# Performance work log

Hardware: AMD Instinct MI355X
Metric: run time of the kernel (lower is better)

## Reference

```python
import jax, jax.numpy as jnp
import numpy as np

B, TOPK, MN = 128, 32, 64
MAX_NODES, H, E = 256, 128, 128
N_ENT, N_REL = 40000, 400


def setup_inputs() -> dict:
    key = jax.random.key(0)
    ks = jax.random.split(key, 11)
    s = 0.02  # weight init scale
    return {
        "node_embeddings": jax.random.normal(ks[0], (B, MAX_NODES + 2, H), jnp.float32),
        "entity_table": jax.random.normal(ks[1], (N_ENT, E), jnp.float32) * s,
        "relation_table": jax.random.normal(ks[2], (N_REL, E), jnp.float32) * s,
        "W_ih": jax.random.normal(ks[3], (3 * H, 2 * E), jnp.float32) * s,
        "W_hh": jax.random.normal(ks[4], (3 * H, H), jnp.float32) * s,
        "b_ih": jax.random.normal(ks[5], (3 * H,), jnp.float32) * s,
        "b_hh": jax.random.normal(ks[6], (3 * H,), jnp.float32) * s,
        "aim_nodes": jax.random.randint(ks[7], (B, TOPK), 0, MAX_NODES),
        "aim_entities": jax.random.randint(ks[8], (B, TOPK), 0, N_ENT),
        "neighbors": jax.random.randint(ks[9], (B, TOPK, MN, 2), 0, MAX_NODES + 2),
        "neighbors_num": jax.random.randint(ks[10], (B, TOPK), 0, MN + 1),
    }


def reference(node_embeddings, entity_table, relation_table, W_ih, W_hh, b_ih, b_hh,
              aim_nodes, aim_entities, neighbors, neighbors_num):
    # Agent.aggregate with use_rnn=True; returns updated node_embeddings.
    b, topk, mn, _ = neighbors.shape
    h_dim = node_embeddings.shape[-1]
    nb_nodes = neighbors[..., 0]      # (B, topk, mn) node positions
    nb_rel = neighbors[..., 1]        # (B, topk, mn) relation ids

    # per-batch gather of hidden states of neighbor nodes -> (B, topk, mn, H)
    h = jnp.take_along_axis(node_embeddings,
                            nb_nodes.reshape(b, topk * mn)[:, :, None],
                            axis=1).reshape(b, topk, mn, h_dim)
    ent = entity_table[aim_entities]          # (B, topk, E)
    rel = relation_table[nb_rel]              # (B, topk, mn, E)
    # GRU input: concat(aim entity embedding broadcast over neighbors, relation emb)
    x = jnp.concatenate(
        [jnp.broadcast_to(ent[:, :, None, :], rel.shape), rel], axis=-1)  # (B,topk,mn,2E)

    # torch GRUCell: gates ordered (r, z, n)
    gi = jnp.einsum('btme,ge->btmg', x, W_ih) + b_ih  # (B,topk,mn,3H)
    gh = jnp.einsum('btmh,gh->btmg', h, W_hh) + b_hh
    i_r, i_z, i_n = jnp.split(gi, 3, axis=-1)
    h_r, h_z, h_n = jnp.split(gh, 3, axis=-1)
    r = jax.nn.sigmoid(i_r + h_r)
    z = jax.nn.sigmoid(i_z + h_z)
    n = jnp.tanh(i_n + r * h_n)
    h_new = (1.0 - z) * n + z * h              # (B,topk,mn,H)

    # masked mean over valid neighbors (masked_fill(0) then sum / max(num,1))
    mask = jnp.arange(mn)[None, None, :] < neighbors_num[:, :, None]
    denom = neighbors_num.astype(h_new.dtype) + (neighbors_num == 0).astype(h_new.dtype)
    upd = jnp.where(mask[..., None], h_new, 0.0).sum(axis=2) / denom[..., None]  # (B,topk,H)

    # scatter updated representations back into the node table
    bidx = jnp.arange(b)[:, None]
    return node_embeddings.at[bidx, aim_nodes].set(upd)
```

## Files before the change

### kernel.cpp

```cpp
#include <hip/hip_runtime.h>

#define BB     128
#define TOPK   32
#define MN     64
#define NODES  258
#define HD     128
#define G3     384
#define NREL   400
#define SEG1_OFF 512
#define SEG2_OFF 4608
#define NROWS_TOT 37632
#define ROWPAD   37632
#define COLSPLIT 3

typedef __bf16 bf16x8 __attribute__((ext_vector_type(8)));
typedef float  f32x4  __attribute__((ext_vector_type(4)));

__device__ inline unsigned short f2bf(float f) {
    unsigned u = __float_as_uint(f);
    u = (u + 0x7fff + ((u >> 16) & 1)) >> 16;
    return (unsigned short)u;
}
__device__ inline float bf2f(unsigned short s) {
    return __uint_as_float(((unsigned)s) << 16);
}
__device__ inline float fsig(float x) {
    float e = __builtin_amdgcn_exp2f(-1.442695041f * x);
    return __builtin_amdgcn_rcpf(1.f + e);
}
__device__ inline float ftanh(float x) {
    x = fminf(15.f, fmaxf(-15.f, x));
    float e = __builtin_amdgcn_exp2f(2.885390082f * x);
    return (e - 1.f) * __builtin_amdgcn_rcpf(e + 1.f);
}

__global__ __launch_bounds__(256) void pack_all(
        const float* __restrict__ node_emb, const float* __restrict__ ent_tab,
        const float* __restrict__ rel_tab, const int* __restrict__ aim_ent,
        unsigned short* __restrict__ A, unsigned short* __restrict__ NE16,
        float* __restrict__ out) {
    int i = blockIdx.x * 256 + threadIdx.x;
    int row = i >> 4, kc = (i & 15) << 3;
    float4 v0 = {0.f,0.f,0.f,0.f}, v1 = {0.f,0.f,0.f,0.f};
    bool isnode = false;
    int n = 0;
    if (row < NREL) {
        const float4* p = (const float4*)(rel_tab + (size_t)row * 128 + kc);
        v0 = p[0]; v1 = p[1];
    } else if (row < SEG1_OFF) {
    } else if (row < SEG2_OFF) {
        const float* e = ent_tab + (size_t)aim_ent[row - SEG1_OFF] * 128 + kc;
        v0 = ((const float4*)e)[0]; v1 = ((const float4*)e)[1];
    } else {
        isnode = true;
        n = row - SEG2_OFF;
        const float4* p = (const float4*)(node_emb + (size_t)n * 128 + kc);
        v0 = p[0]; v1 = p[1];
        float4* o = (float4*)(out + (size_t)n * 128 + kc);
        o[0] = v0; o[1] = v1;
    }
    union { unsigned short s[8]; uint4 v; } u;
    u.s[0]=f2bf(v0.x); u.s[1]=f2bf(v0.y); u.s[2]=f2bf(v0.z); u.s[3]=f2bf(v0.w);
    u.s[4]=f2bf(v1.x); u.s[5]=f2bf(v1.y); u.s[6]=f2bf(v1.z); u.s[7]=f2bf(v1.w);
    *(uint4*)(A + (size_t)row * 128 + kc) = u.v;
    if (isnode) *(uint4*)(NE16 + (size_t)n * 128 + kc) = u.v;
}

__global__ __launch_bounds__(256) void pack_w(
        const float* __restrict__ W_ih, const float* __restrict__ W_hh,
        const float* __restrict__ b_ih, const float* __restrict__ b_hh,
        unsigned short* __restrict__ Wpack, float* __restrict__ biasb) {
    int i = blockIdx.x * 256 + threadIdx.x;
    int s = i / 49152, r = i % 49152;
    int n = r >> 7, k = r & 127;
    float v;
    if (s == 0)      v = W_ih[n * 256 + 128 + k];
    else if (s == 1) v = W_ih[n * 256 + k];
    else             v = W_hh[n * 128 + k];
    Wpack[i] = f2bf(v);
    if (i < 3 * 384) {
        int s2 = i / 384, g = i % 384;
        biasb[i] = (s2 == 0) ? 0.f : (s2 == 1 ? b_ih[g] : b_hh[g]);
    }
}

__global__ __launch_bounds__(256) void mfma_gemm(
        const unsigned short* __restrict__ A, const unsigned short* __restrict__ Wpack,
        const float* __restrict__ biasb, unsigned short* __restrict__ G) {
    __shared__ __align__(16) unsigned short Bs[128 * 128];
    const int tid = threadIdx.x;
    const int w = tid >> 6, lane = tid & 63;
    const int rb = blockIdx.x / COLSPLIT, cs = blockIdx.x % COLSPLIT;
    const int brow = rb * 128;
    const int row0 = brow + w * 32;
    const int seg  = (brow < SEG1_OFF) ? 0 : (brow < SEG2_OFF ? 1 : 2);
    const int limit = (seg == 0) ? NREL : NROWS_TOT;
    const int colbase = cs * 128;
    const unsigned short* Wt = Wpack + (size_t)seg * 49152 + (size_t)colbase * 128;

#pragma unroll
    for (int ii = 0; ii < 8; ++ii) {
        int dst = ii * 256 + tid;
        int g = dst >> 6, rem = dst & 63;
        int qq = rem >> 4, cc = rem & 15;
        int tt = g >> 2, kbb = g & 3;
        uint4 v = *(const uint4*)(Wt + (size_t)(tt * 16 + cc) * 128 + kbb * 32 + qq * 8);
        *(uint4*)(Bs + dst * 8) = v;
    }

    const int q = lane >> 4, c = lane & 15;
    const int koff = q << 3;
    bf16x8 a0[4], a1[4];
    {
        const unsigned short* Ar0 = A + (size_t)(row0 + c) * 128 + koff;
        const unsigned short* Ar1 = Ar0 + 16 * 128;
#pragma unroll
        for (int kb = 0; kb < 4; ++kb) {
            a0[kb] = *(const bf16x8*)(Ar0 + kb * 32);
            a1[kb] = *(const bf16x8*)(Ar1 + kb * 32);
        }
    }
    float bv[8];
#pragma unroll
    for (int t = 0; t < 8; ++t)
        bv[t] = biasb[seg * 384 + colbase + t * 16 + c];

    __syncthreads();

    const int r0 = row0 + q * 4, r1 = r0 + 16;
#pragma unroll 2
    for (int t = 0; t < 8; ++t) {
        bf16x8 bf[4];
#pragma unroll
        for (int kb = 0; kb < 4; ++kb)
            bf[kb] = *(const bf16x8*)(Bs + (size_t)((t * 4 + kb) * 64 + lane) * 8);
        f32x4 acc0 = {0.f,0.f,0.f,0.f}, acc1 = {0.f,0.f,0.f,0.f};
#pragma unroll
        for (int kb = 0; kb < 4; ++kb) {
            acc0 = __builtin_amdgcn_mfma_f32_16x16x32_bf16(a0[kb], bf[kb], acc0, 0, 0, 0);
            acc1 = __builtin_amdgcn_mfma_f32_16x16x32_bf16(a1[kb], bf[kb], acc1, 0, 0, 0);
        }
        const int gc = colbase + t * 16 + c;
#pragma unroll
        for (int i2 = 0; i2 < 4; ++i2) {
            if (r0 + i2 < limit) G[(size_t)(r0 + i2) * 384 + gc] = f2bf(acc0[i2] + bv[t]);
            if (r1 + i2 < limit) G[(size_t)(r1 + i2) * 384 + gc] = f2bf(acc1[i2] + bv[t]);
        }
    }
}

__global__ __launch_bounds__(512) void gru_agg(
        const unsigned short* __restrict__ NE16, const unsigned short* __restrict__ G,
        const int* __restrict__ aim_nodes, const int* __restrict__ neighbors,
        const int* __restrict__ nb_num, float* __restrict__ out) {
    const int bt = blockIdx.x;
    const int b = bt >> 5, t = bt & 31;
    const int tid = threadIdx.x;
    const int h = tid & 127, j = tid >> 7;

    const int myaim = aim_nodes[bt];
    for (int t2 = t + 1; t2 < TOPK; ++t2)
        if (aim_nodes[b * TOPK + t2] == myaim) return;

    __shared__ int2 nbs[MN];
    __shared__ float part[4][128];
    if (tid < MN) nbs[tid] = ((const int2*)(neighbors + (size_t)bt * MN * 2))[tid];
    __syncthreads();

    const size_t erow = (size_t)(SEG1_OFF + bt) * 384;
    const float ge_r = bf2f(G[erow + h]);
    const float ge_z = bf2f(G[erow + 128 + h]);
    const float ge_n = bf2f(G[erow + 256 + h]);

    int num = nb_num[bt];
    num = (num < 0) ? 0 : (num > MN ? MN : num);

    const unsigned short* ghb = G + (size_t)(SEG2_OFF + b * NODES) * 384;
    const unsigned short* heb = NE16 + (size_t)b * NODES * 128;

    float acc = 0.f;
    int m = j;
    for (; m + 4 < num; m += 8) {
        int2 p0 = nbs[m], p1 = nbs[m + 4];
        const unsigned short* gr0 = G + (size_t)p0.y * 384;
        const unsigned short* gh0 = ghb + (size_t)p0.x * 384;
        const unsigned short* gr1 = G + (size_t)p1.y * 384;
        const unsigned short* gh1 = ghb + (size_t)p1.x * 384;
        float ar0 = bf2f(gr0[h]), az0 = bf2f(gr0[128+h]), an0 = bf2f(gr0[256+h]);
        float hr0 = bf2f(gh0[h]), hz0 = bf2f(gh0[128+h]), hn0 = bf2f(gh0[256+h]);
        float hv0 = bf2f(heb[(size_t)p0.x * 128 + h]);
        float ar1 = bf2f(gr1[h]), az1 = bf2f(gr1[128+h]), an1 = bf2f(gr1[256+h]);
        float hr1 = bf2f(gh1[h]), hz1 = bf2f(gh1[128+h]), hn1 = bf2f(gh1[256+h]);
        float hv1 = bf2f(heb[(size_t)p1.x * 128 + h]);
        float r0 = fsig(ge_r + ar0 + hr0);
        float z0 = fsig(ge_z + az0 + hz0);
        float n0 = ftanh(ge_n + an0 + r0 * hn0);
        acc += (1.f - z0) * n0 + z0 * hv0;
        float r1 = fsig(ge_r + ar1 + hr1);
        float z1 = fsig(ge_z + az1 + hz1);
        float n1 = ftanh(ge_n + an1 + r1 * hn1);
        acc += (1.f - z1) * n1 + z1 * hv1;
    }
    if (m < num) {
        int2 p = nbs[m];
        const unsigned short* gr = G + (size_t)p.y * 384;
        const unsigned short* gh = ghb + (size_t)p.x * 384;
        float r = fsig(ge_r + bf2f(gr[h]) + bf2f(gh[h]));
        float z = fsig(ge_z + bf2f(gr[128 + h]) + bf2f(gh[128 + h]));
        float n = ftanh(ge_n + bf2f(gr[256 + h]) + r * bf2f(gh[256 + h]));
        acc += (1.f - z) * n + z * bf2f(heb[(size_t)p.x * 128 + h]);
    }
    part[j][h] = acc;
    __syncthreads();
    if (j == 0) {
        float s = part[0][h] + part[1][h] + part[2][h] + part[3][h];
        const float denom = (num > 0) ? (float)num : 1.f;
        out[((size_t)b * NODES + myaim) * 128 + h] = s * __builtin_amdgcn_rcpf(denom);
    }
}

extern "C" void kernel_launch(void* const* d_in, const int* in_sizes, int n_in,
                              void* d_out, int out_size, void* d_ws, size_t ws_size,
                              hipStream_t stream) {
    const float* node_emb = (const float*)d_in[0];
    const float* ent_tab  = (const float*)d_in[1];
    const float* rel_tab  = (const float*)d_in[2];
    const float* W_ih     = (const float*)d_in[3];
    const float* W_hh     = (const float*)d_in[4];
    const float* b_ih     = (const float*)d_in[5];
    const float* b_hh     = (const float*)d_in[6];
    const int* aim_nodes  = (const int*)d_in[7];
    const int* aim_ent    = (const int*)d_in[8];
    const int* neighbors  = (const int*)d_in[9];
    const int* nb_num     = (const int*)d_in[10];
    float* out = (float*)d_out;

    unsigned short* G     = (unsigned short*)d_ws;
    unsigned short* A     = G + (size_t)NROWS_TOT * 384;
    unsigned short* NE16  = A + (size_t)ROWPAD * 128;
    unsigned short* Wpack = NE16 + (size_t)BB * NODES * 128;
    float*          biasb = (float*)(Wpack + 3 * 384 * 128);

    hipLaunchKernelGGL(pack_all, dim3(ROWPAD * 16 / 256), dim3(256), 0, stream,
                       node_emb, ent_tab, rel_tab, aim_ent, A, NE16, out);
    hipLaunchKernelGGL(pack_w, dim3(3 * 384 * 128 / 256), dim3(256), 0, stream,
                       W_ih, W_hh, b_ih, b_hh, Wpack, biasb);
    hipLaunchKernelGGL(mfma_gemm, dim3((ROWPAD / 128) * COLSPLIT), dim3(256), 0, stream,
                       A, Wpack, biasb, G);
    hipLaunchKernelGGL(gru_agg, dim3(BB * TOPK), dim3(512), 0, stream,
                       NE16, G, aim_nodes, neighbors, nb_num, out);
}
```

Baseline: 151.2 us.

## Merge pack kernels, drop NE16 copy, and vectorize GRU aggregation loads

Fuses the activation pack and weight pack into one prep kernel, which saves a launch and vectorizes the weight conversion to 8 elements per thread. The separate bf16 node-embedding copy (NE16) is dropped and the aggregation reads the hidden state from the A buffer instead. The GRU aggregation kernel is remapped so each lane handles two adjacent hidden units with 32-bit bf16-pair loads, and 8 warps split the neighbors. This halves the number of load instructions but leaves only 64 active lanes per neighbor row, so per-neighbor parallelism changes.

```diff
diff --git a/kernel.cpp b/kernel.cpp
--- a/kernel.cpp
+++ b/kernel.cpp
@@ -4,13 +4,10 @@
 #define TOPK   32
 #define MN     64
 #define NODES  258
-#define HD     128
-#define G3     384
 #define NREL   400
 #define SEG1_OFF 512
 #define SEG2_OFF 4608
 #define NROWS_TOT 37632
-#define ROWPAD   37632
 #define COLSPLIT 3
 
 typedef __bf16 bf16x8 __attribute__((ext_vector_type(8)));
@@ -21,8 +18,11 @@
     u = (u + 0x7fff + ((u >> 16) & 1)) >> 16;
     return (unsigned short)u;
 }
-__device__ inline float bf2f(unsigned short s) {
-    return __uint_as_float(((unsigned)s) << 16);
+__device__ inline float2 up2(unsigned u) {
+    float2 r;
+    r.x = __uint_as_float(u << 16);
+    r.y = __uint_as_float(u & 0xffff0000u);
+    return r;
 }
 __device__ inline float fsig(float x) {
     float e = __builtin_amdgcn_exp2f(-1.442695041f * x);
@@ -34,53 +34,57 @@
     return (e - 1.f) * __builtin_amdgcn_rcpf(e + 1.f);
 }
 
-__global__ __launch_bounds__(256) void pack_all(
+#define REGA_BLOCKS (NROWS_TOT * 16 / 256)
+#define REGB_BLOCKS (147456 / 8 / 256)
+__global__ __launch_bounds__(256) void prep(
         const float* __restrict__ node_emb, const float* __restrict__ ent_tab,
         const float* __restrict__ rel_tab, const int* __restrict__ aim_ent,
-        unsigned short* __restrict__ A, unsigned short* __restrict__ NE16,
-        float* __restrict__ out) {
-    int i = blockIdx.x * 256 + threadIdx.x;
-    int row = i >> 4, kc = (i & 15) << 3;
-    float4 v0 = {0.f,0.f,0.f,0.f}, v1 = {0.f,0.f,0.f,0.f};
-    bool isnode = false;
-    int n = 0;
-    if (row < NREL) {
-        const float4* p = (const float4*)(rel_tab + (size_t)row * 128 + kc);
-        v0 = p[0]; v1 = p[1];
-    } else if (row < SEG1_OFF) {
-    } else if (row < SEG2_OFF) {
-        const float* e = ent_tab + (size_t)aim_ent[row - SEG1_OFF] * 128 + kc;
-        v0 = ((const float4*)e)[0]; v1 = ((const float4*)e)[1];
-    } else {
-        isnode = true;
-        n = row - SEG2_OFF;
-        const float4* p = (const float4*)(node_emb + (size_t)n * 128 + kc);
-        v0 = p[0]; v1 = p[1];
-        float4* o = (float4*)(out + (size_t)n * 128 + kc);
-        o[0] = v0; o[1] = v1;
-    }
-    union { unsigned short s[8]; uint4 v; } u;
-    u.s[0]=f2bf(v0.x); u.s[1]=f2bf(v0.y); u.s[2]=f2bf(v0.z); u.s[3]=f2bf(v0.w);
-    u.s[4]=f2bf(v1.x); u.s[5]=f2bf(v1.y); u.s[6]=f2bf(v1.z); u.s[7]=f2bf(v1.w);
-    *(uint4*)(A + (size_t)row * 128 + kc) = u.v;
-    if (isnode) *(uint4*)(NE16 + (size_t)n * 128 + kc) = u.v;
-}
-
-__global__ __launch_bounds__(256) void pack_w(
         const float* __restrict__ W_ih, const float* __restrict__ W_hh,
         const float* __restrict__ b_ih, const float* __restrict__ b_hh,
-        unsigned short* __restrict__ Wpack, float* __restrict__ biasb) {
-    int i = blockIdx.x * 256 + threadIdx.x;
-    int s = i / 49152, r = i % 49152;
-    int n = r >> 7, k = r & 127;
-    float v;
-    if (s == 0)      v = W_ih[n * 256 + 128 + k];
-    else if (s == 1) v = W_ih[n * 256 + k];
-    else             v = W_hh[n * 128 + k];
-    Wpack[i] = f2bf(v);
-    if (i < 3 * 384) {
-        int s2 = i / 384, g = i % 384;
-        biasb[i] = (s2 == 0) ? 0.f : (s2 == 1 ? b_ih[g] : b_hh[g]);
+        unsigned short* __restrict__ A, unsigned short* __restrict__ Wpack,
+        float* __restrict__ biasb, float* __restrict__ out) {
+    int gid = blockIdx.x * 256 + threadIdx.x;
+    if (blockIdx.x < REGA_BLOCKS) {
+        int row = gid >> 4, kc = (gid & 15) << 3;
+        float4 v0 = {0.f,0.f,0.f,0.f}, v1 = {0.f,0.f,0.f,0.f};
+        if (row < NREL) {
+            const float4* p = (const float4*)(rel_tab + (size_t)row * 128 + kc);
+            v0 = p[0]; v1 = p[1];
+        } else if (row < SEG1_OFF) {
+        } else if (row < SEG2_OFF) {
+            const float* e = ent_tab + (size_t)aim_ent[row - SEG1_OFF] * 128 + kc;
+            v0 = ((const float4*)e)[0]; v1 = ((const float4*)e)[1];
+        } else {
+            int n = row - SEG2_OFF;
+            const float4* p = (const float4*)(node_emb + (size_t)n * 128 + kc);
+            v0 = p[0]; v1 = p[1];
+            float4* o = (float4*)(out + (size_t)n * 128 + kc);
+            o[0] = v0; o[1] = v1;
+        }
+        union { unsigned short s[8]; uint4 v; } u;
+        u.s[0]=f2bf(v0.x); u.s[1]=f2bf(v0.y); u.s[2]=f2bf(v0.z); u.s[3]=f2bf(v0.w);
+        u.s[4]=f2bf(v1.x); u.s[5]=f2bf(v1.y); u.s[6]=f2bf(v1.z); u.s[7]=f2bf(v1.w);
+        *(uint4*)(A + (size_t)row * 128 + kc) = u.v;
+    } else {
+        int rb = gid - REGA_BLOCKS * 256;
+        int e0 = rb * 8;
+        int s = e0 / 49152, r = e0 % 49152;
+        int n = r >> 7, k = r & 127;
+        const float* src = (s == 0) ? (W_ih + n * 256 + 128 + k)
+                         : (s == 1) ? (W_ih + n * 256 + k)
+                                    : (W_hh + n * 128 + k);
+        float4 v0 = ((const float4*)src)[0], v1 = ((const float4*)src)[1];
+        union { unsigned short s[8]; uint4 v; } u;
+        u.s[0]=f2bf(v0.x); u.s[1]=f2bf(v0.y); u.s[2]=f2bf(v0.z); u.s[3]=f2bf(v0.w);
+        u.s[4]=f2bf(v1.x); u.s[5]=f2bf(v1.y); u.s[6]=f2bf(v1.z); u.s[7]=f2bf(v1.w);
+        *(uint4*)(Wpack + e0) = u.v;
+        if (rb < 144) {
+            for (int j = 0; j < 8; ++j) {
+                int e = rb * 8 + j;
+                int s2 = e / 384, g = e % 384;
+                biasb[e] = (s2 == 0) ? 0.f : (s2 == 1 ? b_ih[g] : b_hh[g]);
+            }
+        }
     }
 }
 
@@ -150,72 +154,69 @@
 }
 
 __global__ __launch_bounds__(512) void gru_agg(
-        const unsigned short* __restrict__ NE16, const unsigned short* __restrict__ G,
+        const unsigned short* __restrict__ A, const unsigned short* __restrict__ G,
         const int* __restrict__ aim_nodes, const int* __restrict__ neighbors,
         const int* __restrict__ nb_num, float* __restrict__ out) {
     const int bt = blockIdx.x;
     const int b = bt >> 5, t = bt & 31;
     const int tid = threadIdx.x;
-    const int h = tid & 127, j = tid >> 7;
+    const int w = tid >> 6, lane = tid & 63;
 
     const int myaim = aim_nodes[bt];
     for (int t2 = t + 1; t2 < TOPK; ++t2)
         if (aim_nodes[b * TOPK + t2] == myaim) return;
 
     __shared__ int2 nbs[MN];
-    __shared__ float part[4][128];
-    if (tid < MN) nbs[tid] = ((const int2*)(neighbors + (size_t)bt * MN * 2))[tid];
+    __shared__ float2 part[8][64];
+    if (tid < MN) nbs[tid] = ((const int2*)neighbors)[(size_t)bt * MN + tid];
     __syncthreads();
-
-    const size_t erow = (size_t)(SEG1_OFF + bt) * 384;
-    const float ge_r = bf2f(G[erow + h]);
-    const float ge_z = bf2f(G[erow + 128 + h]);
-    const float ge_n = bf2f(G[erow + 256 + h]);
 
     int num = nb_num[bt];
     num = (num < 0) ? 0 : (num > MN ? MN : num);
 
-    const unsigned short* ghb = G + (size_t)(SEG2_OFF + b * NODES) * 384;
-    const unsigned short* heb = NE16 + (size_t)b * NODES * 128;
-
-    float acc = 0.f;
-    int m = j;
-    for (; m + 4 < num; m += 8) {
-        int2 p0 = nbs[m], p1 = nbs[m + 4];
-        const unsigned short* gr0 = G + (size_t)p0.y * 384;
-        const unsigned short* gh0 = ghb + (size_t)p0.x * 384;
-        const unsigned short* gr1 = G + (size_t)p1.y * 384;
-        const unsigned short* gh1 = ghb + (size_t)p1.x * 384;
-        float ar0 = bf2f(gr0[h]), az0 = bf2f(gr0[128+h]), an0 = bf2f(gr0[256+h]);
-        float hr0 = bf2f(gh0[h]), hz0 = bf2f(gh0[128+h]), hn0 = bf2f(gh0[256+h]);
-        float hv0 = bf2f(heb[(size_t)p0.x * 128 + h]);
-        float ar1 = bf2f(gr1[h]), az1 = bf2f(gr1[128+h]), an1 = bf2f(gr1[256+h]);
-        float hr1 = bf2f(gh1[h]), hz1 = bf2f(gh1[128+h]), hn1 = bf2f(gh1[256+h]);
-        float hv1 = bf2f(heb[(size_t)p1.x * 128 + h]);
-        float r0 = fsig(ge_r + ar0 + hr0);
-        float z0 = fsig(ge_z + az0 + hz0);
-        float n0 = ftanh(ge_n + an0 + r0 * hn0);
-        acc += (1.f - z0) * n0 + z0 * hv0;
-        float r1 = fsig(ge_r + ar1 + hr1);
-        float z1 = fsig(ge_z + az1 + hz1);
-        float n1 = ftanh(ge_n + an1 + r1 * hn1);
-        acc += (1.f - z1) * n1 + z1 * hv1;
-    }
-    if (m < num) {
+    const unsigned short* Gl = G + 2 * lane;
+    const unsigned short* Ge = Gl + (size_t)(SEG1_OFF + bt) * 384;
+    const float2 ge_r = up2(*(const unsigned*)(Ge));
+    const float2 ge_z = up2(*(const unsigned*)(Ge + 128));
+    const float2 ge_n = up2(*(const unsigned*)(Ge + 256));
+
+    const unsigned short* Gh = Gl + ((size_t)SEG2_OFF + (size_t)b * NODES) * 384;
+    const unsigned short* Av = A + ((size_t)SEG2_OFF + (size_t)b * NODES) * 128 + 2 * lane;
+
+    float2 acc = {0.f, 0.f};
+    for (int m = w; m < num; m += 8) {
         int2 p = nbs[m];
-        const unsigned short* gr = G + (size_t)p.y * 384;
-        const unsigned short* gh = ghb + (size_t)p.x * 384;
-        float r = fsig(ge_r + bf2f(gr[h]) + bf2f(gh[h]));
-        float z = fsig(ge_z + bf2f(gr[128 + h]) + bf2f(gh[128 + h]));
-        float n = ftanh(ge_n + bf2f(gr[256 + h]) + r * bf2f(gh[256 + h]));
-        acc += (1.f - z) * n + z * bf2f(heb[(size_t)p.x * 128 + h]);
-    }
-    part[j][h] = acc;
+        const unsigned short* gr = Gl + (size_t)p.y * 384;
+        const unsigned short* gh = Gh + (size_t)p.x * 384;
+        unsigned ur0 = *(const unsigned*)(gr);
+        unsigned ur1 = *(const unsigned*)(gr + 128);
+        unsigned ur2 = *(const unsigned*)(gr + 256);
+        unsigned uh0 = *(const unsigned*)(gh);
+        unsigned uh1 = *(const unsigned*)(gh + 128);
+        unsigned uh2 = *(const unsigned*)(gh + 256);
+        unsigned uv  = *(const unsigned*)(Av + (size_t)p.x * 128);
+        float2 r0 = up2(ur0), r1 = up2(ur1), r2 = up2(ur2);
+        float2 h0 = up2(uh0), h1 = up2(uh1), h2 = up2(uh2);
+        float2 hv = up2(uv);
+        float rx = fsig(ge_r.x + r0.x + h0.x);
+        float zx = fsig(ge_z.x + r1.x + h1.x);
+        float nx = ftanh(ge_n.x + r2.x + rx * h2.x);
+        acc.x += (1.f - zx) * nx + zx * hv.x;
+        float ry = fsig(ge_r.y + r0.y + h0.y);
+        float zy = fsig(ge_z.y + r1.y + h1.y);
+        float ny = ftanh(ge_n.y + r2.y + ry * h2.y);
+        acc.y += (1.f - zy) * ny + zy * hv.y;
+    }
+    part[w][lane] = acc;
     __syncthreads();
-    if (j == 0) {
-        float s = part[0][h] + part[1][h] + part[2][h] + part[3][h];
+    if (tid < 64) {
+        float2 s = part[0][lane];
+#pragma unroll
+        for (int k = 1; k < 8; ++k) { s.x += part[k][lane].x; s.y += part[k][lane].y; }
         const float denom = (num > 0) ? (float)num : 1.f;
-        out[((size_t)b * NODES + myaim) * 128 + h] = s * __builtin_amdgcn_rcpf(denom);
+        const float sc = __builtin_amdgcn_rcpf(denom);
+        float2 r; r.x = s.x * sc; r.y = s.y * sc;
+        *(float2*)(out + ((size_t)b * NODES + myaim) * 128 + 2 * lane) = r;
     }
 }
 
@@ -237,16 +238,14 @@
 
     unsigned short* G     = (unsigned short*)d_ws;
     unsigned short* A     = G + (size_t)NROWS_TOT * 384;
-    unsigned short* NE16  = A + (size_t)ROWPAD * 128;
-    unsigned short* Wpack = NE16 + (size_t)BB * NODES * 128;
+    unsigned short* Wpack = A + (size_t)NROWS_TOT * 128;
     float*          biasb = (float*)(Wpack + 3 * 384 * 128);
 
-    hipLaunchKernelGGL(pack_all, dim3(ROWPAD * 16 / 256), dim3(256), 0, stream,
-                       node_emb, ent_tab, rel_tab, aim_ent, A, NE16, out);
-    hipLaunchKernelGGL(pack_w, dim3(3 * 384 * 128 / 256), dim3(256), 0, stream,
-                       W_ih, W_hh, b_ih, b_hh, Wpack, biasb);
-    hipLaunchKernelGGL(mfma_gemm, dim3((ROWPAD / 128) * COLSPLIT), dim3(256), 0, stream,
+    hipLaunchKernelGGL(prep, dim3(REGA_BLOCKS + REGB_BLOCKS), dim3(256), 0, stream,
+                       node_emb, ent_tab, rel_tab, aim_ent, W_ih, W_hh, b_ih, b_hh,
+                       A, Wpack, biasb, out);
+    hipLaunchKernelGGL(mfma_gemm, dim3((NROWS_TOT / 128) * COLSPLIT), dim3(256), 0, stream,
                        A, Wpack, biasb, G);
     hipLaunchKernelGGL(gru_agg, dim3(BB * TOPK), dim3(512), 0, stream,
-                       NE16, G, aim_nodes, neighbors, nb_num, out);
-}
+                       A, G, aim_nodes, neighbors, nb_num, out);
+}
```

New measurement: 146.4 us. 3.1% less time.
